# Kernel tuning notes

Measured on AMD Instinct MI355X. Metric: run time of the kernel, lower is better.

The kernel has to match this reference:

```python
import jax, jax.numpy as jnp
import numpy as np

HEADS = 8
DIM_HEAD = 64
BATCH = 2  # classifier-free-guidance batch
LORA_SCALE = 1.0


def setup_inputs() -> dict:
    key = jax.random.key(0)
    ks = jax.random.split(key, 14)
    D, R = 512, 4
    BF, N = 32, 1024  # batch*frames, spatial tokens
    g = lambda k, shape, s: jax.random.normal(k, shape, dtype=jnp.float32) * s
    return {
        "hidden_states": g(ks[0], (BF, N, D), 1.0),
        "Wq": g(ks[1], (D, D), 0.02),
        "Wk": g(ks[2], (D, D), 0.02),
        "Wv": g(ks[3], (D, D), 0.02),
        "q_down": g(ks[4], (D, R), 0.25),
        "q_up": g(ks[5], (R, D), 0.02),
        "k_down": g(ks[6], (D, R), 0.25),
        "k_up": g(ks[7], (R, D), 0.02),
        "v_down": g(ks[8], (D, R), 0.25),
        "v_up": g(ks[9], (R, D), 0.02),
        "Wo": g(ks[10], (D, D), 0.02),
        "bo": jnp.zeros((D,), jnp.float32),
        "o_down": g(ks[11], (D, R), 0.25),
        "o_up": g(ks[12], (R, D), 0.02),
    }


def reference(hidden_states, Wq, Wk, Wv, q_down, q_up, k_down, k_up,
              v_down, v_up, Wo, bo, o_down, o_up):
    BF, N, C = hidden_states.shape
    F = BF // BATCH  # video_length
    inner = HEADS * DIM_HEAD

    # LoRA-augmented QKV projections (self-attention: context == hidden_states)
    q = hidden_states @ Wq + LORA_SCALE * ((hidden_states @ q_down) @ q_up)
    k = hidden_states @ Wk + LORA_SCALE * ((hidden_states @ k_down) @ k_up)
    v = hidden_states @ Wv + LORA_SCALE * ((hidden_states @ v_down) @ v_up)

    # previous-frame gather: frame f attends to frame max(f-1, 0)
    prev = jnp.concatenate([jnp.zeros((1,), jnp.int32),
                            jnp.arange(F - 1, dtype=jnp.int32)])
    k = k.reshape(BATCH, F, N, inner)[:, prev].reshape(BF, N, inner)
    v = v.reshape(BATCH, F, N, inner)[:, prev].reshape(BF, N, inner)

    def to_heads(t):  # (BF, N, inner) -> (BF*H, N, dh)
        return t.reshape(BF, N, HEADS, DIM_HEAD).transpose(0, 2, 1, 3)\
                .reshape(BF * HEADS, N, DIM_HEAD)

    qh, kh, vh = to_heads(q), to_heads(k), to_heads(v)

    scores = jnp.einsum('bid,bjd->bij', qh, kh) * (DIM_HEAD ** -0.5)
    probs = jax.nn.softmax(scores, axis=-1)
    h = jnp.einsum('bij,bjd->bid', probs, vh)

    # heads back to channel dim
    h = h.reshape(BF, HEADS, N, DIM_HEAD).transpose(0, 2, 1, 3).reshape(BF, N, inner)

    # output projection (with bias) + LoRA on the pre-projection activations
    return h @ Wo + bo + LORA_SCALE * ((h @ o_down) @ o_up)
```

## Files before the change

### kernel.cpp

```cpp
#include <hip/hip_runtime.h>
#include <hip/hip_bf16.h>
#include <math.h>

#define D512 512
#define NTOK 1024
#define QSCALE 0.1803368801111137f

typedef __attribute__((ext_vector_type(8))) short short8;
typedef __attribute__((ext_vector_type(4))) float f32x4;
typedef __attribute__((ext_vector_type(16))) float f32x16;
typedef __attribute__((ext_vector_type(4))) unsigned int u32x4;
typedef unsigned short ushort;

__device__ inline ushort f2bf(float x) {
    union { float f; unsigned u; } a; a.f = x;
    unsigned r = a.u + 0x7FFF + ((a.u >> 16) & 1);
    return (ushort)(r >> 16);
}

__device__ inline unsigned cvtpk(float a, float b) {
    unsigned r;
    asm volatile("v_cvt_pk_bf16_f32 %0, %1, %2" : "=v"(r) : "v"(a), "v"(b));
    return r;
}

__device__ inline void plswap(unsigned &a, unsigned &b) {
    asm volatile("v_permlane32_swap_b32 %0, %1" : "+v"(a), "+v"(b));
}

#define GLL16(src, dst) __builtin_amdgcn_global_load_lds( \
    (const __attribute__((address_space(1))) unsigned int*)(src), \
    (__attribute__((address_space(3))) unsigned int*)(dst), 16, 0, 0)

__global__ __launch_bounds__(256) void cvt_bf16(
    const float* __restrict__ in, ushort* __restrict__ out)
{
    const int idx = blockIdx.x * 256 + threadIdx.x;
    float4 a = ((const float4*)in)[idx * 2];
    float4 b = ((const float4*)in)[idx * 2 + 1];
    short8 s;
    s[0] = f2bf(a.x); s[1] = f2bf(a.y); s[2] = f2bf(a.z); s[3] = f2bf(a.w);
    s[4] = f2bf(b.x); s[5] = f2bf(b.y); s[6] = f2bf(b.z); s[7] = f2bf(b.w);
    *(short8*)&out[(size_t)idx * 8] = s;
}

__global__ __launch_bounds__(256) void fold_weights_T(
    const float* __restrict__ Wq, const float* __restrict__ Wk,
    const float* __restrict__ Wv, const float* __restrict__ Wo,
    const float* __restrict__ qd, const float* __restrict__ qu,
    const float* __restrict__ kd, const float* __restrict__ ku,
    const float* __restrict__ vd, const float* __restrict__ vu,
    const float* __restrict__ od, const float* __restrict__ ou,
    ushort* __restrict__ out)
{
    const int which = blockIdx.y;
    const float *W, *dn, *up;
    if (which == 0)      { W = Wq; dn = qd; up = qu; }
    else if (which == 1) { W = Wk; dn = kd; up = ku; }
    else if (which == 2) { W = Wv; dn = vd; up = vu; }
    else                 { W = Wo; dn = od; up = ou; }

    const int td = (blockIdx.x >> 3) * 64;
    const int te = (blockIdx.x & 7) * 64;
    __shared__ float T[64][65];
    const int r4 = threadIdx.x >> 6;
    const int c  = threadIdx.x & 63;

    #pragma unroll
    for (int i = 0; i < 16; ++i) {
        int row = i * 4 + r4;
        T[row][c] = W[(size_t)(td + row) * 512 + te + c];
    }
    __syncthreads();
    #pragma unroll
    for (int i = 0; i < 16; ++i) {
        int e = te + i * 4 + r4;
        int d = td + c;
        float s = T[c][i * 4 + r4];
        #pragma unroll
        for (int r = 0; r < 4; ++r) s += dn[d * 4 + r] * up[r * 512 + e];
        out[(size_t)which * 262144 + (size_t)e * 512 + d] = f2bf(s);
    }
}

#define SWZT(r, c) ((((r) * 128) + (c)) ^ (((r) & 7) << 3))

template<int QKV>
__global__ __launch_bounds__(256) void gemm_mfma(
    const ushort* __restrict__ A, const ushort* __restrict__ BT,
    const float* __restrict__ bias, float* __restrict__ Co,
    ushort* __restrict__ qb, ushort* __restrict__ kb, ushort* __restrict__ vtb)
{
    __shared__ ushort smem[16384];

    const int tid = threadIdx.x;
    const int w = tid >> 6, l = tid & 63;
    const int l15 = l & 15, l4 = l >> 4;

    const int wg = blockIdx.x;
    const int rxcd = wg & 7, t = wg >> 3;
    const int NX = QKV ? 12 : 4;
    const int xb = t % NX, yh = t / NX;
    const int yb = (yh << 3) | rxcd;
    const int m0 = yb * 128;
    const int n0 = xb * 128;

    const int srow = l >> 2;
    const int scol = (l & 3) * 8;
    const ushort* Asrc = A  + (size_t)(m0 + w * 32 + srow) * 512 + scol;
    const ushort* Bsrc = BT + (size_t)(n0 + w * 32 + srow) * 512 + scol;

    const int wm = (w >> 1) * 64, wn = (w & 1) * 64;

    f32x4 acc[4][4] = {};

    {
        ushort* AsW = smem + w * 1024;
        ushort* BsW = smem + 4096 + w * 1024;
        GLL16(Asrc, AsW);            GLL16(Asrc + 16 * 512, AsW + 512);
        GLL16(Bsrc, BsW);            GLL16(Bsrc + 16 * 512, BsW + 512);
    }
    __syncthreads();

    int cur = 0;
    for (int k0 = 0; k0 < 512; k0 += 32) {
        if (k0 < 480) {
            ushort* AsW = smem + (cur ^ 1) * 8192 + w * 1024;
            ushort* BsW = smem + (cur ^ 1) * 8192 + 4096 + w * 1024;
            GLL16(Asrc + k0 + 32, AsW);
            GLL16(Asrc + k0 + 32 + 16 * 512, AsW + 512);
            GLL16(Bsrc + k0 + 32, BsW);
            GLL16(Bsrc + k0 + 32 + 16 * 512, BsW + 512);
        }
        const ushort* As = smem + cur * 8192;
        const ushort* Bs = smem + cur * 8192 + 4096;

        short8 bfr[4];
        #pragma unroll
        for (int ni = 0; ni < 4; ++ni)
            bfr[ni] = *(const short8*)&Bs[(wn + ni * 16 + l15) * 32 + l4 * 8];
        __builtin_amdgcn_s_setprio(1);
        #pragma unroll
        for (int mi = 0; mi < 4; ++mi) {
            short8 af = *(const short8*)&As[(wm + mi * 16 + l15) * 32 + l4 * 8];
            #pragma unroll
            for (int ni = 0; ni < 4; ++ni)
                acc[mi][ni] = __builtin_amdgcn_mfma_f32_16x16x32_bf16(
                    af, bfr[ni], acc[mi][ni], 0, 0, 0);
        }
        __builtin_amdgcn_s_setprio(0);
        __syncthreads();
        cur ^= 1;
    }

    if (QKV) {
        const int which = xb >> 2;
        if (which < 2) {
            const float sc = which ? 1.0f : QSCALE;
            ushort* dst = which ? kb : qb;
            const int headbase = (n0 & 511) >> 6;
            #pragma unroll
            for (int h = 0; h < 2; ++h) {
                if (wm == h * 64) {
                    #pragma unroll
                    for (int mi = 0; mi < 4; ++mi)
                        #pragma unroll
                        for (int j = 0; j < 4; ++j) {
                            const int r = mi * 16 + l4 * 4 + j;
                            #pragma unroll
                            for (int ni = 0; ni < 4; ++ni) {
                                const int c = wn + ni * 16 + l15;
                                smem[SWZT(r, c)] = f2bf(acc[mi][ni][j] * sc);
                            }
                        }
                }
                __syncthreads();
                const int rr2 = tid >> 4;
                const int cc2 = (tid & 15) * 8;
                const int chunk = cc2 >> 6;
                const int d0 = cc2 & 63;
                #pragma unroll
                for (int s = 0; s < 4; ++s) {
                    const int r = s * 16 + rr2;
                    const int token = m0 + h * 64 + r;
                    const size_t off = (((size_t)(token >> 10) * 8 + headbase + chunk)
                                        * NTOK + (token & 1023)) * 64 + d0;
                    *(u32x4*)&dst[off] = *(const u32x4*)&smem[SWZT(r, cc2)];
                }
                if (h == 0) __syncthreads();
            }
        } else {
            #pragma unroll
            for (int mi = 0; mi < 4; ++mi) {
                const int rowb = m0 + wm + mi * 16 + l4 * 4;
                const int nn = rowb & 1023;
                const int bf8 = (rowb >> 10) * 8;
                #pragma unroll
                for (int ni = 0; ni < 4; ++ni) {
                    const int col = (n0 & 511) + wn + ni * 16 + l15;
                    const int d = col & 63, head = (col >> 6) & 7;
                    unsigned w0 = cvtpk(acc[mi][ni][0], acc[mi][ni][1]);
                    unsigned w1 = cvtpk(acc[mi][ni][2], acc[mi][ni][3]);
                    *(unsigned long long*)&vtb[((size_t)(bf8 + head) * 64 + d) * NTOK + nn] =
                        (unsigned long long)w0 | ((unsigned long long)w1 << 32);
                }
            }
        }
    } else {
        float bvals[4];
        #pragma unroll
        for (int ni = 0; ni < 4; ++ni)
            bvals[ni] = bias[n0 + wn + ni * 16 + l15];
        #pragma unroll
        for (int mi = 0; mi < 4; ++mi)
            #pragma unroll
            for (int j = 0; j < 4; ++j) {
                const int row = m0 + wm + mi * 16 + l4 * 4 + j;
                #pragma unroll
                for (int ni = 0; ni < 4; ++ni) {
                    const int col = n0 + wn + ni * 16 + l15;
                    Co[(size_t)row * 512 + col] = acc[mi][ni][j] + bvals[ni];
                }
            }
    }
}

#define SWZ(r, c) ((((r) * 64) + (c)) ^ (((r) & 7) << 3))

#define SOFTPACK(sv0, sv1, lsum, pa) { \
    unsigned pk[2][4][2]; \
    float ls = 0.f; \
    _Pragma("unroll") \
    for (int rq = 0; rq < 4; ++rq) { \
        float p0 = __builtin_amdgcn_exp2f(sv0[4 * rq + 0]); \
        float p1 = __builtin_amdgcn_exp2f(sv0[4 * rq + 1]); \
        float p2 = __builtin_amdgcn_exp2f(sv0[4 * rq + 2]); \
        float p3 = __builtin_amdgcn_exp2f(sv0[4 * rq + 3]); \
        ls += (p0 + p1) + (p2 + p3); \
        pk[0][rq][0] = cvtpk(p0, p1); \
        pk[0][rq][1] = cvtpk(p2, p3); \
        float q0 = __builtin_amdgcn_exp2f(sv1[4 * rq + 0]); \
        float q1 = __builtin_amdgcn_exp2f(sv1[4 * rq + 1]); \
        float q2 = __builtin_amdgcn_exp2f(sv1[4 * rq + 2]); \
        float q3 = __builtin_amdgcn_exp2f(sv1[4 * rq + 3]); \
        ls += (q0 + q1) + (q2 + q3); \
        pk[1][rq][0] = cvtpk(q0, q1); \
        pk[1][rq][1] = cvtpk(q2, q3); \
    } \
    lsum += ls; \
    _Pragma("unroll") \
    for (int ks = 0; ks < 4; ++ks) { \
        const int kt2 = ks >> 1, q2i = ks & 1; \
        unsigned a0 = pk[kt2][2 * q2i][0], b0 = pk[kt2][2 * q2i + 1][0]; \
        unsigned a1 = pk[kt2][2 * q2i][1], b1 = pk[kt2][2 * q2i + 1][1]; \
        plswap(a0, b0); \
        plswap(a1, b1); \
        pa[ks].u[0] = a0; pa[ks].u[1] = a1; \
        pa[ks].u[2] = b0; pa[ks].u[3] = b1; \
    } }

__global__ __launch_bounds__(256, 2) void attn_mfma32(
    const ushort* __restrict__ qb, const ushort* __restrict__ kb,
    const ushort* __restrict__ vtb, ushort* __restrict__ hb)
{
    __shared__ ushort smem[16384];

    const int tid = threadIdx.x;
    const int w = tid >> 6, l = tid & 63;
    const int l31 = l & 31, hi = l >> 5;
    const int lr = l >> 3, lc = l & 7;

    const int wg = blockIdx.x;
    const int rxcd = wg & 7, t = wg >> 3;
    const int qblk = t & 3;
    const int bh = ((t >> 2) << 3) | rxcd;

    const size_t qbase = (size_t)bh * 65536;
    const int src_bh = ((bh >> 3) & 15) ? bh - 8 : bh;
    const size_t kvbase = (size_t)src_bh * 65536;

    const int qrowA = qblk * 256 + w * 32 + l31;
    const ushort* qpA = qb + qbase + (size_t)qrowA * 64 + hi * 8;
    const ushort* qpB = qpA + 128 * 64;
    short8 qfA[4], qfB[4];
    #pragma unroll
    for (int dq = 0; dq < 4; ++dq) {
        qfA[dq] = *(const short8*)(qpA + dq * 16);
        qfB[dq] = *(const short8*)(qpB + dq * 16);
    }

    f32x16 accA0 = {}, accA1 = {}, accB0 = {}, accB1 = {};
    float lsumA = 0.f, lsumB = 0.f;

    const int r0 = w * 16 + lr;
    const int ck8 = (lc ^ lr) * 8;

#define STAGE_KV(ktv, b) { \
    ushort* KD = smem + (b) * 8192 + w * 1024; \
    ushort* VD = smem + (b) * 8192 + 4096 + w * 1024; \
    GLL16(kb  + kvbase + (size_t)((ktv) * 64 + r0)     * 64 + ck8, KD); \
    GLL16(kb  + kvbase + (size_t)((ktv) * 64 + r0 + 8) * 64 + ck8, KD + 512); \
    GLL16(vtb + kvbase + (size_t)r0       * 1024 + (ktv) * 64 + ck8, VD); \
    GLL16(vtb + kvbase + (size_t)(r0 + 8) * 1024 + (ktv) * 64 + ck8, VD + 512); }

    STAGE_KV(0, 0);
    __syncthreads();

    int cur = 0;
    for (int kt = 0; kt < 16; ++kt) {
        if (kt < 15) STAGE_KV(kt + 1, cur ^ 1);
        const ushort* Ks = smem + cur * 8192;
        const ushort* Vt = smem + cur * 8192 + 4096;

        f32x16 svA0 = {}, svA1 = {}, svB0 = {}, svB1 = {};
        __builtin_amdgcn_s_setprio(1);
        #pragma unroll
        for (int dq = 0; dq < 4; ++dq) {
            short8 kf0 = *(const short8*)&Ks[SWZ(l31,      dq * 16 + hi * 8)];
            short8 kf1 = *(const short8*)&Ks[SWZ(32 + l31, dq * 16 + hi * 8)];
            svA0 = __builtin_amdgcn_mfma_f32_32x32x16_bf16(kf0, qfA[dq], svA0, 0, 0, 0);
            svA1 = __builtin_amdgcn_mfma_f32_32x32x16_bf16(kf1, qfA[dq], svA1, 0, 0, 0);
            svB0 = __builtin_amdgcn_mfma_f32_32x32x16_bf16(kf0, qfB[dq], svB0, 0, 0, 0);
            svB1 = __builtin_amdgcn_mfma_f32_32x32x16_bf16(kf1, qfB[dq], svB1, 0, 0, 0);
        }
        __builtin_amdgcn_s_setprio(0);

        union { u32x4 u; short8 s; } paA[4], paB[4];
        SOFTPACK(svA0, svA1, lsumA, paA);
        SOFTPACK(svB0, svB1, lsumB, paB);

        __builtin_amdgcn_s_setprio(1);
        #pragma unroll
        for (int ks = 0; ks < 4; ++ks) {
            short8 vf0 = *(const short8*)&Vt[SWZ(l31,      ks * 16 + hi * 8)];
            short8 vf1 = *(const short8*)&Vt[SWZ(32 + l31, ks * 16 + hi * 8)];
            accA0 = __builtin_amdgcn_mfma_f32_32x32x16_bf16(vf0, paA[ks].s, accA0, 0, 0, 0);
            accA1 = __builtin_amdgcn_mfma_f32_32x32x16_bf16(vf1, paA[ks].s, accA1, 0, 0, 0);
            accB0 = __builtin_amdgcn_mfma_f32_32x32x16_bf16(vf0, paB[ks].s, accB0, 0, 0, 0);
            accB1 = __builtin_amdgcn_mfma_f32_32x32x16_bf16(vf1, paB[ks].s, accB1, 0, 0, 0);
        }
        __builtin_amdgcn_s_setprio(0);

        __syncthreads();
        cur ^= 1;
    }
#undef STAGE_KV

    {
        unsigned au = __float_as_uint(lsumA), bu = au;
        plswap(au, bu);
        lsumA = __uint_as_float(au) + __uint_as_float(bu);
        unsigned cu2 = __float_as_uint(lsumB), du = cu2;
        plswap(cu2, du);
        lsumB = __uint_as_float(cu2) + __uint_as_float(du);
    }

    ushort* tw = smem + w * 2048;
    const int q2 = l >> 1, ch = (l & 1) * 32;
    {
        const float inv = 1.f / lsumA;
        #pragma unroll
        for (int r = 0; r < 16; ++r) {
            const int d = (r & 3) + 8 * (r >> 2) + 4 * hi;
            tw[SWZ(l31, d)]      = f2bf(accA0[r] * inv);
            tw[SWZ(l31, 32 + d)] = f2bf(accA1[r] * inv);
        }
        const int hrow = qblk * 256 + w * 32 + q2;
        ushort* gdst = hb + ((size_t)(bh >> 3) * NTOK + hrow) * D512 + (bh & 7) * 64 + ch;
        #pragma unroll
        for (int c = 0; c < 4; ++c)
            *(u32x4*)(gdst + c * 8) = *(const u32x4*)&tw[SWZ(q2, ch + c * 8)];
    }
    __builtin_amdgcn_s_waitcnt(0);
    {
        const float inv = 1.f / lsumB;
        #pragma unroll
        for (int r = 0; r < 16; ++r) {
            const int d = (r & 3) + 8 * (r >> 2) + 4 * hi;
            tw[SWZ(l31, d)]      = f2bf(accB0[r] * inv);
            tw[SWZ(l31, 32 + d)] = f2bf(accB1[r] * inv);
        }
        const int hrow = qblk * 256 + 128 + w * 32 + q2;
        ushort* gdst = hb + ((size_t)(bh >> 3) * NTOK + hrow) * D512 + (bh & 7) * 64 + ch;
        #pragma unroll
        for (int c = 0; c < 4; ++c)
            *(u32x4*)(gdst + c * 8) = *(const u32x4*)&tw[SWZ(q2, ch + c * 8)];
    }
}

extern "C" void kernel_launch(void* const* d_in, const int* in_sizes, int n_in,
                              void* d_out, int out_size, void* d_ws, size_t ws_size,
                              hipStream_t stream)
{
    const float* hs = (const float*)d_in[0];
    const float* Wq = (const float*)d_in[1];
    const float* Wk = (const float*)d_in[2];
    const float* Wv = (const float*)d_in[3];
    const float* qd = (const float*)d_in[4];
    const float* qu = (const float*)d_in[5];
    const float* kd = (const float*)d_in[6];
    const float* ku = (const float*)d_in[7];
    const float* vd = (const float*)d_in[8];
    const float* vu = (const float*)d_in[9];
    const float* Wo = (const float*)d_in[10];
    const float* bo = (const float*)d_in[11];
    const float* od = (const float*)d_in[12];
    const float* ou = (const float*)d_in[13];

    ushort* wsb = (ushort*)d_ws;
    ushort* WT  = wsb;
    ushort* hsb = wsb + 1048576;
    ushort* qb  = hsb + 16777216;
    ushort* kb  = qb  + 16777216;
    ushort* vtb = kb  + 16777216;
    ushort* hbb = vtb + 16777216;

    float* out = (float*)d_out;

    cvt_bf16<<<dim3(8192), 256, 0, stream>>>(hs, hsb);
    fold_weights_T<<<dim3(64, 4), 256, 0, stream>>>(
        Wq, Wk, Wv, Wo, qd, qu, kd, ku, vd, vu, od, ou, WT);

    gemm_mfma<1><<<dim3(3072), 256, 0, stream>>>(
        hsb, WT, nullptr, nullptr, qb, kb, vtb);

    attn_mfma32<<<dim3(1024), 256, 0, stream>>>(qb, kb, vtb, hbb);

    gemm_mfma<0><<<dim3(1024), 256, 0, stream>>>(
        hbb, WT + 786432, bo, out, nullptr, nullptr, nullptr);
}
```

Before: 202.6 us.

## Split attention into single-wave workgroups with 32-key tiles and no barriers

The attention kernel is restructured from 256-thread workgroups covering 256 query rows into 64-thread single-wave workgroups covering 64 query rows, launched as 4096 blocks. Each wave stages its own 32-key K/V tiles into a smaller double-buffered LDS region with a new V swizzle, and uses vmcnt waits instead of __syncthreads. This removes block-wide barriers and raises scheduling flexibility. In exchange, each K/V tile is loaded by four times as many workgroups, which adds global/L2 traffic, and the per-tile MFMA work shrinks.

```diff
diff --git a/kernel.cpp b/kernel.cpp
--- a/kernel.cpp
+++ b/kernel.cpp
@@ -225,63 +225,54 @@
     }
 }
 
-#define SWZ(r, c) ((((r) * 64) + (c)) ^ (((r) & 7) << 3))
-
-#define SOFTPACK(sv0, sv1, lsum, pa) { \
-    unsigned pk[2][4][2]; \
+#define SWZ(r, c)  ((((r) * 64) + (c)) ^ (((r) & 7) << 3))
+#define VSWZ(r, c) ((((r) * 32) + (c)) ^ ((((r) >> 1) & 3) << 3))
+
+#define SOFTPACK32(sv, lsum, pa) { \
+    unsigned pk[4][2]; \
     float ls = 0.f; \
     _Pragma("unroll") \
     for (int rq = 0; rq < 4; ++rq) { \
-        float p0 = __builtin_amdgcn_exp2f(sv0[4 * rq + 0]); \
-        float p1 = __builtin_amdgcn_exp2f(sv0[4 * rq + 1]); \
-        float p2 = __builtin_amdgcn_exp2f(sv0[4 * rq + 2]); \
-        float p3 = __builtin_amdgcn_exp2f(sv0[4 * rq + 3]); \
+        float p0 = __builtin_amdgcn_exp2f(sv[4 * rq + 0]); \
+        float p1 = __builtin_amdgcn_exp2f(sv[4 * rq + 1]); \
+        float p2 = __builtin_amdgcn_exp2f(sv[4 * rq + 2]); \
+        float p3 = __builtin_amdgcn_exp2f(sv[4 * rq + 3]); \
         ls += (p0 + p1) + (p2 + p3); \
-        pk[0][rq][0] = cvtpk(p0, p1); \
-        pk[0][rq][1] = cvtpk(p2, p3); \
-        float q0 = __builtin_amdgcn_exp2f(sv1[4 * rq + 0]); \
-        float q1 = __builtin_amdgcn_exp2f(sv1[4 * rq + 1]); \
-        float q2 = __builtin_amdgcn_exp2f(sv1[4 * rq + 2]); \
-        float q3 = __builtin_amdgcn_exp2f(sv1[4 * rq + 3]); \
-        ls += (q0 + q1) + (q2 + q3); \
-        pk[1][rq][0] = cvtpk(q0, q1); \
-        pk[1][rq][1] = cvtpk(q2, q3); \
+        pk[rq][0] = cvtpk(p0, p1); \
+        pk[rq][1] = cvtpk(p2, p3); \
     } \
     lsum += ls; \
     _Pragma("unroll") \
-    for (int ks = 0; ks < 4; ++ks) { \
-        const int kt2 = ks >> 1, q2i = ks & 1; \
-        unsigned a0 = pk[kt2][2 * q2i][0], b0 = pk[kt2][2 * q2i + 1][0]; \
-        unsigned a1 = pk[kt2][2 * q2i][1], b1 = pk[kt2][2 * q2i + 1][1]; \
+    for (int kc = 0; kc < 2; ++kc) { \
+        unsigned a0 = pk[2 * kc][0], b0 = pk[2 * kc + 1][0]; \
+        unsigned a1 = pk[2 * kc][1], b1 = pk[2 * kc + 1][1]; \
         plswap(a0, b0); \
         plswap(a1, b1); \
-        pa[ks].u[0] = a0; pa[ks].u[1] = a1; \
-        pa[ks].u[2] = b0; pa[ks].u[3] = b1; \
+        pa[kc].u[0] = a0; pa[kc].u[1] = a1; \
+        pa[kc].u[2] = b0; pa[kc].u[3] = b1; \
     } }
 
-__global__ __launch_bounds__(256, 2) void attn_mfma32(
+__global__ __launch_bounds__(64, 2) void attn_wave(
     const ushort* __restrict__ qb, const ushort* __restrict__ kb,
     const ushort* __restrict__ vtb, ushort* __restrict__ hb)
 {
-    __shared__ ushort smem[16384];
-
-    const int tid = threadIdx.x;
-    const int w = tid >> 6, l = tid & 63;
+    __shared__ ushort smem[8192];
+
+    const int l = threadIdx.x;
     const int l31 = l & 31, hi = l >> 5;
-    const int lr = l >> 3, lc = l & 7;
 
     const int wg = blockIdx.x;
     const int rxcd = wg & 7, t = wg >> 3;
-    const int qblk = t & 3;
-    const int bh = ((t >> 2) << 3) | rxcd;
+    const int qt = t & 15;
+    const int bh = ((t >> 4) << 3) | rxcd;
 
     const size_t qbase = (size_t)bh * 65536;
     const int src_bh = ((bh >> 3) & 15) ? bh - 8 : bh;
     const size_t kvbase = (size_t)src_bh * 65536;
 
-    const int qrowA = qblk * 256 + w * 32 + l31;
+    const int qrowA = qt * 64 + l31;
     const ushort* qpA = qb + qbase + (size_t)qrowA * 64 + hi * 8;
-    const ushort* qpB = qpA + 128 * 64;
+    const ushort* qpB = qpA + 32 * 64;
     short8 qfA[4], qfB[4];
     #pragma unroll
     for (int dq = 0; dq < 4; ++dq) {
@@ -292,59 +283,62 @@
     f32x16 accA0 = {}, accA1 = {}, accB0 = {}, accB1 = {};
     float lsumA = 0.f, lsumB = 0.f;
 
-    const int r0 = w * 16 + lr;
-    const int ck8 = (lc ^ lr) * 8;
-
-#define STAGE_KV(ktv, b) { \
-    ushort* KD = smem + (b) * 8192 + w * 1024; \
-    ushort* VD = smem + (b) * 8192 + 4096 + w * 1024; \
-    GLL16(kb  + kvbase + (size_t)((ktv) * 64 + r0)     * 64 + ck8, KD); \
-    GLL16(kb  + kvbase + (size_t)((ktv) * 64 + r0 + 8) * 64 + ck8, KD + 512); \
-    GLL16(vtb + kvbase + (size_t)r0       * 1024 + (ktv) * 64 + ck8, VD); \
-    GLL16(vtb + kvbase + (size_t)(r0 + 8) * 1024 + (ktv) * 64 + ck8, VD + 512); }
-
-    STAGE_KV(0, 0);
-    __syncthreads();
+    const int klr = l >> 3, klc = l & 7;
+    const int kck = (klc ^ klr) * 8;
+    const int vro = l >> 2, vch = l & 3;
+
+#define STAGE32(ktv, b) { \
+    ushort* KD = smem + (b) * 4096; \
+    ushort* VD = smem + (b) * 4096 + 2048; \
+    const ushort* ksrc = kb + kvbase + (size_t)((ktv) * 32) * 64; \
+    _Pragma("unroll") \
+    for (int j = 0; j < 4; ++j) \
+        GLL16(ksrc + (size_t)(j * 8 + klr) * 64 + kck, KD + j * 512); \
+    _Pragma("unroll") \
+    for (int j = 0; j < 4; ++j) { \
+        const int rv = j * 16 + vro; \
+        GLL16(vtb + kvbase + (size_t)rv * 1024 + (ktv) * 32 \
+              + ((vch ^ ((rv >> 1) & 3)) * 8), VD + j * 512); \
+    } }
+
+    STAGE32(0, 0);
 
     int cur = 0;
-    for (int kt = 0; kt < 16; ++kt) {
-        if (kt < 15) STAGE_KV(kt + 1, cur ^ 1);
-        const ushort* Ks = smem + cur * 8192;
-        const ushort* Vt = smem + cur * 8192 + 4096;
-
-        f32x16 svA0 = {}, svA1 = {}, svB0 = {}, svB1 = {};
+    for (int kt = 0; kt < 32; ++kt) {
+        asm volatile("s_waitcnt vmcnt(0)" ::: "memory");
+        __builtin_amdgcn_sched_barrier(0);
+        if (kt < 31) STAGE32(kt + 1, cur ^ 1);
+        const ushort* Ks = smem + cur * 4096;
+        const ushort* Vt = smem + cur * 4096 + 2048;
+
+        f32x16 svA = {}, svB = {};
         __builtin_amdgcn_s_setprio(1);
         #pragma unroll
         for (int dq = 0; dq < 4; ++dq) {
-            short8 kf0 = *(const short8*)&Ks[SWZ(l31,      dq * 16 + hi * 8)];
-            short8 kf1 = *(const short8*)&Ks[SWZ(32 + l31, dq * 16 + hi * 8)];
-            svA0 = __builtin_amdgcn_mfma_f32_32x32x16_bf16(kf0, qfA[dq], svA0, 0, 0, 0);
-            svA1 = __builtin_amdgcn_mfma_f32_32x32x16_bf16(kf1, qfA[dq], svA1, 0, 0, 0);
-            svB0 = __builtin_amdgcn_mfma_f32_32x32x16_bf16(kf0, qfB[dq], svB0, 0, 0, 0);
-            svB1 = __builtin_amdgcn_mfma_f32_32x32x16_bf16(kf1, qfB[dq], svB1, 0, 0, 0);
+            short8 kf = *(const short8*)&Ks[SWZ(l31, dq * 16 + hi * 8)];
+            svA = __builtin_amdgcn_mfma_f32_32x32x16_bf16(kf, qfA[dq], svA, 0, 0, 0);
+            svB = __builtin_amdgcn_mfma_f32_32x32x16_bf16(kf, qfB[dq], svB, 0, 0, 0);
         }
         __builtin_amdgcn_s_setprio(0);
 
-        union { u32x4 u; short8 s; } paA[4], paB[4];
-        SOFTPACK(svA0, svA1, lsumA, paA);
-        SOFTPACK(svB0, svB1, lsumB, paB);
+        union { u32x4 u; short8 s; } paA[2], paB[2];
+        SOFTPACK32(svA, lsumA, paA);
+        SOFTPACK32(svB, lsumB, paB);
 
         __builtin_amdgcn_s_setprio(1);
         #pragma unroll
-        for (int ks = 0; ks < 4; ++ks) {
-            short8 vf0 = *(const short8*)&Vt[SWZ(l31,      ks * 16 + hi * 8)];
-            short8 vf1 = *(const short8*)&Vt[SWZ(32 + l31, ks * 16 + hi * 8)];
-            accA0 = __builtin_amdgcn_mfma_f32_32x32x16_bf16(vf0, paA[ks].s, accA0, 0, 0, 0);
-            accA1 = __builtin_amdgcn_mfma_f32_32x32x16_bf16(vf1, paA[ks].s, accA1, 0, 0, 0);
-            accB0 = __builtin_amdgcn_mfma_f32_32x32x16_bf16(vf0, paB[ks].s, accB0, 0, 0, 0);
-            accB1 = __builtin_amdgcn_mfma_f32_32x32x16_bf16(vf1, paB[ks].s, accB1, 0, 0, 0);
+        for (int kc = 0; kc < 2; ++kc) {
+            short8 vf0 = *(const short8*)&Vt[VSWZ(l31,      kc * 16 + hi * 8)];
+            short8 vf1 = *(const short8*)&Vt[VSWZ(32 + l31, kc * 16 + hi * 8)];
+            accA0 = __builtin_amdgcn_mfma_f32_32x32x16_bf16(vf0, paA[kc].s, accA0, 0, 0, 0);
+            accA1 = __builtin_amdgcn_mfma_f32_32x32x16_bf16(vf1, paA[kc].s, accA1, 0, 0, 0);
+            accB0 = __builtin_amdgcn_mfma_f32_32x32x16_bf16(vf0, paB[kc].s, accB0, 0, 0, 0);
+            accB1 = __builtin_amdgcn_mfma_f32_32x32x16_bf16(vf1, paB[kc].s, accB1, 0, 0, 0);
         }
         __builtin_amdgcn_s_setprio(0);
-
-        __syncthreads();
         cur ^= 1;
     }
-#undef STAGE_KV
+#undef STAGE32
 
     {
         unsigned au = __float_as_uint(lsumA), bu = au;
@@ -355,7 +349,7 @@
         lsumB = __uint_as_float(cu2) + __uint_as_float(du);
     }
 
-    ushort* tw = smem + w * 2048;
+    ushort* tw = smem;
     const int q2 = l >> 1, ch = (l & 1) * 32;
     {
         const float inv = 1.f / lsumA;
@@ -365,7 +359,7 @@
             tw[SWZ(l31, d)]      = f2bf(accA0[r] * inv);
             tw[SWZ(l31, 32 + d)] = f2bf(accA1[r] * inv);
         }
-        const int hrow = qblk * 256 + w * 32 + q2;
+        const int hrow = qt * 64 + q2;
         ushort* gdst = hb + ((size_t)(bh >> 3) * NTOK + hrow) * D512 + (bh & 7) * 64 + ch;
         #pragma unroll
         for (int c = 0; c < 4; ++c)
@@ -380,7 +374,7 @@
             tw[SWZ(l31, d)]      = f2bf(accB0[r] * inv);
             tw[SWZ(l31, 32 + d)] = f2bf(accB1[r] * inv);
         }
-        const int hrow = qblk * 256 + 128 + w * 32 + q2;
+        const int hrow = qt * 64 + 32 + q2;
         ushort* gdst = hb + ((size_t)(bh >> 3) * NTOK + hrow) * D512 + (bh & 7) * 64 + ch;
         #pragma unroll
         for (int c = 0; c < 4; ++c)
@@ -424,7 +418,7 @@
     gemm_mfma<1><<<dim3(3072), 256, 0, stream>>>(
         hsb, WT, nullptr, nullptr, qb, kb, vtb);
 
-    attn_mfma32<<<dim3(1024), 256, 0, stream>>>(qb, kb, vtb, hbb);
+    attn_wave<<<dim3(4096), 64, 0, stream>>>(qb, kb, vtb, hbb);
 
     gemm_mfma<0><<<dim3(1024), 256, 0, stream>>>(
         hbb, WT + 786432, bo, out, nullptr, nullptr, nullptr);
```

Result: slower. 218.3 us (+7.8%).
